# Kernel tuning notes

Measured on AMD Instinct MI355X. Metric: run time of the kernel, lower is better.

Reference implementation:

```python
import jax, jax.numpy as jnp
import numpy as np

# Winograd F(4x4, 3x3) transform matrices (wincnn convention, as in jiecaoyu/winograd)
BT = jnp.array([
    [4.,  0., -5.,  0., 1., 0.],
    [0., -4., -4.,  1., 1., 0.],
    [0.,  4., -4., -1., 1., 0.],
    [0., -2., -1.,  2., 1., 0.],
    [0.,  2., -1., -2., 1., 0.],
    [0.,  4.,  0., -5., 0., 1.]], dtype=jnp.float32)  # [6,6]
AT = jnp.array([
    [1., 1.,  1., 1.,  1., 0.],
    [0., 1., -1., 2., -2., 0.],
    [0., 1.,  1., 4.,  4., 0.],
    [0., 1., -1., 8., -8., 1.]], dtype=jnp.float32)  # [4,6]

KERNEL = 3
PAD = 1
GROUPS = 1
TILE_IN = 6   # input_tile_size
TILE_OUT = 4  # output_tile_size


def setup_inputs() -> dict:
    key = jax.random.key(0)
    k1, k2, k3 = jax.random.split(key, 3)
    N, Cin, H, W = 16, 64, 128, 128
    Cout = 64
    x = jax.random.normal(k1, (N, Cin, H, W), dtype=jnp.float32)
    # weight is stored in the Winograd (6x6 spectral) domain, as in the module
    weight = jax.random.normal(k2, (Cout, Cin // GROUPS, TILE_IN, TILE_IN), dtype=jnp.float32) * 0.01
    bias = jax.random.normal(k3, (Cout,), dtype=jnp.float32) * 0.01
    return {"x": x, "weight": weight, "bias": bias}


def reference(x, weight, bias):
    N, Cin, H0, W0 = x.shape
    Cout = weight.shape[0]
    g = GROUPS
    # conv padding
    x = jnp.pad(x, ((0, 0), (0, 0), (PAD, PAD), (PAD, PAD)))
    H = x.shape[2]
    out_w = H - KERNEL + 1
    # pad so output width is a multiple of the output tile size
    extra = (-out_w) % TILE_OUT
    if extra:
        x = jnp.pad(x, ((0, 0), (0, 0), (0, extra), (0, extra)))
    nt = (x.shape[2] - TILE_IN) // TILE_OUT + 1  # tiles per spatial dim
    # extract overlapping 6x6 tiles with stride 4 (the torch unfold)
    idx = jnp.arange(nt)[:, None] * TILE_OUT + jnp.arange(TILE_IN)[None, :]  # [nt,6]
    tiles = x[:, :, idx]                 # [N,C,nt,6,Wp]
    tiles = tiles[:, :, :, :, idx]       # [N,C,nt,6,nt,6]
    # input transform: V = BT @ d @ BT^T per tile -> [N,C,nt,nt,6,6]
    V = jnp.einsum('ai,ncpiqj,bj->ncpqab', BT, tiles, BT)
    # grouped spectral GEMM over input channels
    Vg = V.reshape(N, g, Cin // g, nt, nt, TILE_IN, TILE_IN)
    Wg = weight.reshape(g, Cout // g, Cin // g, TILE_IN, TILE_IN)
    M = jnp.einsum('goiab,ngipqab->ngopqab', Wg, Vg)
    M = M.reshape(N, Cout, nt, nt, TILE_IN, TILE_IN)
    # output transform: Y = AT @ M @ AT^T per tile -> [N,O,nt,nt,4,4]
    Y = jnp.einsum('xa,nopqab,yb->nopqxy', AT, M, AT)
    # stitch tiles back: [N,O,nt,4,nt,4] -> [N,O,nt*4,nt*4]
    y = Y.transpose(0, 1, 2, 4, 3, 5).reshape(N, Cout, nt * TILE_OUT, nt * TILE_OUT)
    y = y + bias[None, :, None, None]
    # crop the extra padding
    y = y[:, :, :out_w, :out_w]
    return y
```

## Files before the change

### kernel.cpp

```cpp
#include <hip/hip_runtime.h>
#include <stdint.h>

typedef __attribute__((ext_vector_type(4))) float f32x4;
typedef __attribute__((ext_vector_type(2))) float f32x2;
typedef __attribute__((ext_vector_type(8))) short s16x8;

#define WB_BYTES 294912

__device__ __forceinline__ short f2bf(float f) {
    uint32_t u = __builtin_bit_cast(uint32_t, f);
    u = u + 0x7FFFu + ((u >> 16) & 1u);
    return (short)(u >> 16);
}

__device__ __forceinline__ f32x4 load4u(const float* p) {
    f32x4 v;
    __builtin_memcpy(&v, p, 16);
    return v;
}

__global__ __launch_bounds__(256) void wtrans(const float* __restrict__ wf, short* __restrict__ wb) {
    int tid = blockIdx.x * 256 + threadIdx.x;
    const float* src = wf + tid * 36;
    float w[36];
#pragma unroll
    for (int i = 0; i < 9; i++) {
        f32x4 v = *(const f32x4*)(src + 4 * i);
        w[4*i+0] = v[0]; w[4*i+1] = v[1]; w[4*i+2] = v[2]; w[4*i+3] = v[3];
    }
#pragma unroll
    for (int ab = 0; ab < 36; ab++) wb[ab * 4096 + tid] = f2bf(w[ab]);
}

#define XCI 440
__global__ __launch_bounds__(1024) void wino_fused(const float* __restrict__ x,
                                                   const short* __restrict__ wb,
                                                   const float* __restrict__ bias,
                                                   float* __restrict__ out) {
    __shared__ __align__(16) float SM[39680];
    float* X0 = SM;
    float* X1 = SM + 14080;
    short* Vs = (short*)(SM + 28160);
    float* P0 = SM;
    float* P1 = SM + 16384;

    int t = threadIdx.x;
    int lane = t & 63;
    int w = t >> 6;
    int cog = w >> 2;
    int grp = w & 3;
    int sh = grp >> 1;
    int bh = grp & 1;
    int lo = lane & 15;
    int kq = lane >> 4;

    int ci_t = t & 31;
    int tl_t = (t >> 5) & 15;
    int s2_t = t >> 9;
    int tp = tl_t >> 2, tq = tl_t & 3;

    int tci[4], trow[4], tc4[4];
#pragma unroll
    for (int i = 0; i < 4; i++) {
        int s = i * 1024 + t;
        int ci = s / 108;
        int rem = s - ci * 108;
        int row = rem / 6;
        tci[i] = ci; trow[i] = row; tc4[i] = rem - row * 6;
    }
    bool v3 = t < 384;

    float bv = bias[cog * 16 + kq * 4 + grp];

    f32x4 acc[9];
#pragma unroll
    for (int i = 0; i < 9; i++) acc[i] = (f32x4){0.f, 0.f, 0.f, 0.f};

    f32x4 L[4];

    auto issueLoads = [&](int vb, int r) {
        int n = vb >> 6, sb = vb & 63;
        int row0 = (sb >> 3) * 16 - 1;
        int gc0 = (sb & 7) * 16 - 1;
        const float* xb = x + (size_t)n * 64 * 16384;
#pragma unroll
        for (int i = 0; i < 4; i++) {
            if (i < 3 || v3) {
                int gr = row0 + trow[i];
                int gc = gc0 + 4 * tc4[i];
                f32x4 v = (f32x4){0.f, 0.f, 0.f, 0.f};
                if ((unsigned)gr < 128u) {
                    const float* rowp = xb + (size_t)((r * 32 + tci[i]) * 128 + gr) * 128;
                    if (gc >= 0 && gc <= 124) {
                        v = load4u(rowp + gc);
                    } else {
                        if ((unsigned)(gc + 0) < 128u) v[0] = rowp[gc + 0];
                        if ((unsigned)(gc + 1) < 128u) v[1] = rowp[gc + 1];
                        if ((unsigned)(gc + 2) < 128u) v[2] = rowp[gc + 2];
                        if ((unsigned)(gc + 3) < 128u) v[3] = rowp[gc + 3];
                    }
                }
                L[i] = v;
            }
        }
    };

    auto writeX = [&](float* Xb) {
#pragma unroll
        for (int i = 0; i < 4; i++) {
            if (i < 3 || v3)
                *(f32x4*)&Xb[tci[i] * XCI + trow[i] * 24 + tc4[i] * 4] = L[i];
        }
    };

    auto transform = [&](const float* Xbuf) {
        const float* Xb = Xbuf + ci_t * XCI + tp * 96 + tq * 4;
        f32x4 ra[5]; f32x2 rb[5];
#pragma unroll
        for (int k = 0; k < 5; k++) {
            int off = (s2_t + k) * 24;
            ra[k] = *(const f32x4*)(Xb + off);
            rb[k] = *(const f32x2*)(Xb + off + 4);
        }
        float Ua[3][6];
#pragma unroll
        for (int c = 0; c < 6; c++) {
            float e0 = (c < 4) ? ra[0][c] : rb[0][c - 4];
            float e1 = (c < 4) ? ra[1][c] : rb[1][c - 4];
            float e2 = (c < 4) ? ra[2][c] : rb[2][c - 4];
            float e3 = (c < 4) ? ra[3][c] : rb[3][c - 4];
            float e4 = (c < 4) ? ra[4][c] : rb[4][c - 4];
            if (s2_t == 0) {
                float e = fmaf(-4.f, e2, e4);
                float f = fmaf(-4.f, e1, e3);
                Ua[0][c] = fmaf(4.f, e0 - e2, e4 - e2);
                Ua[1][c] = e + f;
                Ua[2][c] = e - f;
            } else {
                float g = e3 - e1;
                float h = e2 - e0;
                Ua[0][c] = fmaf(2.f, h, g);
                Ua[1][c] = fmaf(-2.f, h, g);
                Ua[2][c] = fmaf(4.f, e0 - e2, e4 - e2);
            }
        }
        short* vb = Vs + tl_t * 40 + ci_t;
#pragma unroll
        for (int ar = 0; ar < 3; ar++) {
            float m0 = Ua[ar][0], m1 = Ua[ar][1], m2 = Ua[ar][2];
            float m3 = Ua[ar][3], m4 = Ua[ar][4], m5 = Ua[ar][5];
            float e = fmaf(-4.f, m2, m4);
            float f = fmaf(-4.f, m1, m3);
            float g = m4 - m2;
            float h = m3 - m1;
            int base = (s2_t * 3 + ar) * 6;
            vb[(base + 0) * 640] = f2bf(fmaf(4.f, m0 - m2, g));
            vb[(base + 1) * 640] = f2bf(e + f);
            vb[(base + 2) * 640] = f2bf(e - f);
            vb[(base + 3) * 640] = f2bf(fmaf(2.f, h, g));
            vb[(base + 4) * 640] = f2bf(fmaf(-2.f, h, g));
            vb[(base + 5) * 640] = f2bf(fmaf(4.f, m1 - m3, m5 - m3));
        }
    };

    auto gemmStep = [&](int r) {
        const short* wb_base = wb + (cog * 16 + lo) * 64 + r * 32 + kq * 8;
        const short* v_base = Vs + lo * 40 + kq * 8;
#pragma unroll
        for (int ar = 0; ar < 3; ar++) {
#pragma unroll
            for (int br = 0; br < 3; br++) {
                int ab = (3 * sh + ar) * 6 + 3 * bh + br;
                s16x8 a0 = *(const s16x8*)(wb_base + ab * 4096);
                s16x8 b0 = *(const s16x8*)(v_base + ab * 640);
                acc[ar * 3 + br] = __builtin_amdgcn_mfma_f32_16x16x32_bf16(a0, b0, acc[ar * 3 + br], 0, 0, 0);
            }
        }
    };

    int vb0 = blockIdx.x * 4;
    issueLoads(vb0, 0);

    for (int it = 0; it < 4; ++it) {
        int vb = vb0 + it;
        int n = vb >> 6, sb = vb & 63;
        int p0_ = (sb >> 3) * 4;
        int q0_ = (sb & 7) * 4;

        writeX(X0);
        __syncthreads();
        issueLoads(vb, 1);
        transform(X0);
        writeX(X1);
        __syncthreads();
        gemmStep(0);
        __syncthreads();
        transform(X1);
        __syncthreads();
        gemmStep(1);
        __syncthreads();

        if (it < 3) issueLoads(vb + 1, 0);

        int p = p0_ + (lo >> 2);
        int q = q0_ + (lo & 3);
        float* Pown = (sh == 0) ? P0 : P1;

        if (bh == 0) {
#pragma unroll
            for (int rr = 0; rr < 4; rr++) {
                float z[4][3];
#pragma unroll
                for (int br = 0; br < 3; br++) {
                    float ma = acc[br][rr], mb = acc[3 + br][rr], mc = acc[6 + br][rr];
                    if (sh == 0) {
                        float s1 = mb + mc, d1 = mb - mc;
                        z[0][br] = ma + s1; z[1][br] = d1; z[2][br] = s1; z[3][br] = d1;
                    } else {
                        float sv = ma + mb, dv = ma - mb;
                        z[0][br] = sv; z[1][br] = 2.f * dv; z[2][br] = 4.f * sv;
                        z[3][br] = fmaf(8.f, dv, mc);
                    }
                }
#pragma unroll
                for (int xr = 0; xr < 4; xr++) {
                    float s1 = z[xr][1] + z[xr][2], d1 = z[xr][1] - z[xr][2];
                    f32x4 y;
                    y[0] = z[xr][0] + s1; y[1] = d1; y[2] = s1; y[3] = d1;
                    *(f32x4*)&Pown[cog * 4096 + (rr * 4 + xr) * 256 + lane * 4] = y;
                }
            }
        }
        __syncthreads();
        if (bh == 1) {
#pragma unroll
            for (int rr = 0; rr < 4; rr++) {
                float z[4][3];
#pragma unroll
                for (int br = 0; br < 3; br++) {
                    float ma = acc[br][rr], mb = acc[3 + br][rr], mc = acc[6 + br][rr];
                    if (sh == 0) {
                        float s1 = mb + mc, d1 = mb - mc;
                        z[0][br] = ma + s1; z[1][br] = d1; z[2][br] = s1; z[3][br] = d1;
                    } else {
                        float sv = ma + mb, dv = ma - mb;
                        z[0][br] = sv; z[1][br] = 2.f * dv; z[2][br] = 4.f * sv;
                        z[3][br] = fmaf(8.f, dv, mc);
                    }
                }
#pragma unroll
                for (int xr = 0; xr < 4; xr++) {
                    float s2 = z[xr][0] + z[xr][1], d2 = z[xr][0] - z[xr][1];
                    f32x4 y;
                    y[0] = s2; y[1] = 2.f * d2; y[2] = 4.f * s2;
                    y[3] = fmaf(8.f, d2, z[xr][2]);
                    float* pp = &Pown[cog * 4096 + (rr * 4 + xr) * 256 + lane * 4];
                    f32x4 old = *(const f32x4*)pp;
                    *(f32x4*)pp = old + y;
                }
            }
        }
        __syncthreads();
        {
            int rr = grp;
            int co = cog * 16 + kq * 4 + rr;
            float* ob = out + ((size_t)(n * 64 + co) * 128 + 4 * p) * 128 + 4 * q;
#pragma unroll
            for (int xr = 0; xr < 4; xr++) {
                int idx = cog * 4096 + (rr * 4 + xr) * 256 + lane * 4;
                f32x4 a0 = *(const f32x4*)&P0[idx];
                f32x4 a1 = *(const f32x4*)&P1[idx];
                f32x4 y;
                y[0] = a0[0] + a1[0] + bv;
                y[1] = a0[1] + a1[1] + bv;
                y[2] = a0[2] + a1[2] + bv;
                y[3] = a0[3] + a1[3] + bv;
                *(f32x4*)(ob + xr * 128) = y;
            }
        }
#pragma unroll
        for (int i = 0; i < 9; i++) acc[i] = (f32x4){0.f, 0.f, 0.f, 0.f};
        if (it < 3) __syncthreads();
    }
}

extern "C" void kernel_launch(void* const* d_in, const int* in_sizes, int n_in,
                              void* d_out, int out_size, void* d_ws, size_t ws_size,
                              hipStream_t stream) {
    const float* x    = (const float*)d_in[0];
    const float* wf   = (const float*)d_in[1];
    const float* bias = (const float*)d_in[2];
    float* out = (float*)d_out;

    if (ws_size < WB_BYTES) return;
    short* wb = (short*)d_ws;

    wtrans<<<16, 256, 0, stream>>>(wf, wb);
    wino_fused<<<256, 1024, 0, stream>>>(x, wb, bias, out);
}
```

Before: 224.1 us.

## One spatial block per workgroup, drop double-buffered prefetch, add interior fast path

New measurement: 187.1 us. -16.5%, faster.

```diff
diff --git a/kernel.cpp b/kernel.cpp
--- a/kernel.cpp
+++ b/kernel.cpp
@@ -32,15 +32,14 @@
     for (int ab = 0; ab < 36; ab++) wb[ab * 4096 + tid] = f2bf(w[ab]);
 }
 
-#define XCI 440
+#define XCI 436
 __global__ __launch_bounds__(1024) void wino_fused(const float* __restrict__ x,
                                                    const short* __restrict__ wb,
                                                    const float* __restrict__ bias,
                                                    float* __restrict__ out) {
-    __shared__ __align__(16) float SM[39680];
-    float* X0 = SM;
-    float* X1 = SM + 14080;
-    short* Vs = (short*)(SM + 28160);
+    __shared__ __align__(16) float SM[32768];
+    float* X = SM;
+    short* Vs = (short*)(SM + 13952);
     float* P0 = SM;
     float* P1 = SM + 16384;
 
@@ -59,16 +58,15 @@
     int s2_t = t >> 9;
     int tp = tl_t >> 2, tq = tl_t & 3;
 
-    int tci[4], trow[4], tc4[4];
-#pragma unroll
-    for (int i = 0; i < 4; i++) {
-        int s = i * 1024 + t;
-        int ci = s / 108;
-        int rem = s - ci * 108;
-        int row = rem / 6;
-        tci[i] = ci; trow[i] = row; tc4[i] = rem - row * 6;
-    }
-    bool v3 = t < 384;
+    int b = blockIdx.x;
+    int n = b >> 6, sb = b & 63;
+    int p0_ = (sb >> 3) * 4;
+    int q0_ = (sb & 7) * 4;
+    const float* xb = x + (size_t)n * 64 * 16384;
+    int row0 = 4 * p0_ - 1;
+    int gc0 = 4 * q0_ - 1;
+    int sr = sb >> 3, sc = sb & 7;
+    bool interior = (sr >= 1) & (sr <= 6) & (sc >= 1) & (sc <= 6);
 
     float bv = bias[cog * 16 + kq * 4 + grp];
 
@@ -76,211 +74,194 @@
 #pragma unroll
     for (int i = 0; i < 9; i++) acc[i] = (f32x4){0.f, 0.f, 0.f, 0.f};
 
-    f32x4 L[4];
-
-    auto issueLoads = [&](int vb, int r) {
-        int n = vb >> 6, sb = vb & 63;
-        int row0 = (sb >> 3) * 16 - 1;
-        int gc0 = (sb & 7) * 16 - 1;
-        const float* xb = x + (size_t)n * 64 * 16384;
-#pragma unroll
-        for (int i = 0; i < 4; i++) {
-            if (i < 3 || v3) {
-                int gr = row0 + trow[i];
-                int gc = gc0 + 4 * tc4[i];
-                f32x4 v = (f32x4){0.f, 0.f, 0.f, 0.f};
-                if ((unsigned)gr < 128u) {
-                    const float* rowp = xb + (size_t)((r * 32 + tci[i]) * 128 + gr) * 128;
-                    if (gc >= 0 && gc <= 124) {
-                        v = load4u(rowp + gc);
-                    } else {
-                        if ((unsigned)(gc + 0) < 128u) v[0] = rowp[gc + 0];
-                        if ((unsigned)(gc + 1) < 128u) v[1] = rowp[gc + 1];
-                        if ((unsigned)(gc + 2) < 128u) v[2] = rowp[gc + 2];
-                        if ((unsigned)(gc + 3) < 128u) v[3] = rowp[gc + 3];
+#pragma unroll
+    for (int r = 0; r < 2; r++) {
+        const float* xrb = xb + (size_t)r * 32 * 16384;
+        if (interior) {
+#pragma unroll
+            for (int i = 0; i < 4; i++) {
+                if (i < 3 || t < 384) {
+                    int s = i * 1024 + t;
+                    int ci = s / 108;
+                    int rem = s - ci * 108;
+                    int row = rem / 6;
+                    int c4 = rem - row * 6;
+                    f32x4 v = load4u(xrb + (size_t)(ci * 128 + row0 + row) * 128 + (gc0 + 4 * c4));
+                    *(f32x4*)&X[ci * XCI + row * 24 + c4 * 4] = v;
+                }
+            }
+        } else {
+#pragma unroll
+            for (int i = 0; i < 4; i++) {
+                if (i < 3 || t < 384) {
+                    int s = i * 1024 + t;
+                    int ci = s / 108;
+                    int rem = s - ci * 108;
+                    int row = rem / 6;
+                    int c4 = rem - row * 6;
+                    int gr = row0 + row;
+                    int gc = gc0 + 4 * c4;
+                    f32x4 v = (f32x4){0.f, 0.f, 0.f, 0.f};
+                    if ((unsigned)gr < 128u) {
+                        const float* rowp = xrb + (size_t)(ci * 128 + gr) * 128;
+                        if (gc >= 0 && gc <= 124) {
+                            v = load4u(rowp + gc);
+                        } else {
+                            if ((unsigned)(gc + 0) < 128u) v[0] = rowp[gc + 0];
+                            if ((unsigned)(gc + 1) < 128u) v[1] = rowp[gc + 1];
+                            if ((unsigned)(gc + 2) < 128u) v[2] = rowp[gc + 2];
+                            if ((unsigned)(gc + 3) < 128u) v[3] = rowp[gc + 3];
+                        }
                     }
-                }
-                L[i] = v;
-            }
-        }
-    };
-
-    auto writeX = [&](float* Xb) {
-#pragma unroll
-        for (int i = 0; i < 4; i++) {
-            if (i < 3 || v3)
-                *(f32x4*)&Xb[tci[i] * XCI + trow[i] * 24 + tc4[i] * 4] = L[i];
-        }
-    };
-
-    auto transform = [&](const float* Xbuf) {
-        const float* Xb = Xbuf + ci_t * XCI + tp * 96 + tq * 4;
-        f32x4 ra[5]; f32x2 rb[5];
-#pragma unroll
-        for (int k = 0; k < 5; k++) {
-            int off = (s2_t + k) * 24;
-            ra[k] = *(const f32x4*)(Xb + off);
-            rb[k] = *(const f32x2*)(Xb + off + 4);
-        }
-        float Ua[3][6];
-#pragma unroll
-        for (int c = 0; c < 6; c++) {
-            float e0 = (c < 4) ? ra[0][c] : rb[0][c - 4];
-            float e1 = (c < 4) ? ra[1][c] : rb[1][c - 4];
-            float e2 = (c < 4) ? ra[2][c] : rb[2][c - 4];
-            float e3 = (c < 4) ? ra[3][c] : rb[3][c - 4];
-            float e4 = (c < 4) ? ra[4][c] : rb[4][c - 4];
-            if (s2_t == 0) {
-                float e = fmaf(-4.f, e2, e4);
-                float f = fmaf(-4.f, e1, e3);
-                Ua[0][c] = fmaf(4.f, e0 - e2, e4 - e2);
-                Ua[1][c] = e + f;
-                Ua[2][c] = e - f;
-            } else {
-                float g = e3 - e1;
-                float h = e2 - e0;
-                Ua[0][c] = fmaf(2.f, h, g);
-                Ua[1][c] = fmaf(-2.f, h, g);
-                Ua[2][c] = fmaf(4.f, e0 - e2, e4 - e2);
-            }
-        }
-        short* vb = Vs + tl_t * 40 + ci_t;
-#pragma unroll
-        for (int ar = 0; ar < 3; ar++) {
-            float m0 = Ua[ar][0], m1 = Ua[ar][1], m2 = Ua[ar][2];
-            float m3 = Ua[ar][3], m4 = Ua[ar][4], m5 = Ua[ar][5];
-            float e = fmaf(-4.f, m2, m4);
-            float f = fmaf(-4.f, m1, m3);
-            float g = m4 - m2;
-            float h = m3 - m1;
-            int base = (s2_t * 3 + ar) * 6;
-            vb[(base + 0) * 640] = f2bf(fmaf(4.f, m0 - m2, g));
-            vb[(base + 1) * 640] = f2bf(e + f);
-            vb[(base + 2) * 640] = f2bf(e - f);
-            vb[(base + 3) * 640] = f2bf(fmaf(2.f, h, g));
-            vb[(base + 4) * 640] = f2bf(fmaf(-2.f, h, g));
-            vb[(base + 5) * 640] = f2bf(fmaf(4.f, m1 - m3, m5 - m3));
-        }
-    };
-
-    auto gemmStep = [&](int r) {
-        const short* wb_base = wb + (cog * 16 + lo) * 64 + r * 32 + kq * 8;
-        const short* v_base = Vs + lo * 40 + kq * 8;
-#pragma unroll
-        for (int ar = 0; ar < 3; ar++) {
+                    *(f32x4*)&X[ci * XCI + row * 24 + c4 * 4] = v;
+                }
+            }
+        }
+        __syncthreads();
+
+        {
+            const float* Xb = X + ci_t * XCI + tp * 96 + tq * 4;
+            f32x4 ra[5]; f32x2 rb[5];
+#pragma unroll
+            for (int k = 0; k < 5; k++) {
+                int off = (s2_t + k) * 24;
+                ra[k] = *(const f32x4*)(Xb + off);
+                rb[k] = *(const f32x2*)(Xb + off + 4);
+            }
+            float Ua[3][6];
+#pragma unroll
+            for (int c = 0; c < 6; c++) {
+                float e0 = (c < 4) ? ra[0][c] : rb[0][c - 4];
+                float e1 = (c < 4) ? ra[1][c] : rb[1][c - 4];
+                float e2 = (c < 4) ? ra[2][c] : rb[2][c - 4];
+                float e3 = (c < 4) ? ra[3][c] : rb[3][c - 4];
+                float e4 = (c < 4) ? ra[4][c] : rb[4][c - 4];
+                if (s2_t == 0) {
+                    float e = fmaf(-4.f, e2, e4);
+                    float f = fmaf(-4.f, e1, e3);
+                    Ua[0][c] = fmaf(4.f, e0 - e2, e4 - e2);
+                    Ua[1][c] = e + f;
+                    Ua[2][c] = e - f;
+                } else {
+                    float g = e3 - e1;
+                    float h = e2 - e0;
+                    Ua[0][c] = fmaf(2.f, h, g);
+                    Ua[1][c] = fmaf(-2.f, h, g);
+                    Ua[2][c] = fmaf(4.f, e0 - e2, e4 - e2);
+                }
+            }
+            short* vb = Vs + tl_t * 40 + ci_t;
+#pragma unroll
+            for (int ar = 0; ar < 3; ar++) {
+                float m0 = Ua[ar][0], m1 = Ua[ar][1], m2 = Ua[ar][2];
+                float m3 = Ua[ar][3], m4 = Ua[ar][4], m5 = Ua[ar][5];
+                float e = fmaf(-4.f, m2, m4);
+                float f = fmaf(-4.f, m1, m3);
+                float g = m4 - m2;
+                float h = m3 - m1;
+                int base = (s2_t * 3 + ar) * 6;
+                vb[(base + 0) * 640] = f2bf(fmaf(4.f, m0 - m2, g));
+                vb[(base + 1) * 640] = f2bf(e + f);
+                vb[(base + 2) * 640] = f2bf(e - f);
+                vb[(base + 3) * 640] = f2bf(fmaf(2.f, h, g));
+                vb[(base + 4) * 640] = f2bf(fmaf(-2.f, h, g));
+                vb[(base + 5) * 640] = f2bf(fmaf(4.f, m1 - m3, m5 - m3));
+            }
+        }
+        __syncthreads();
+
+        {
+            const short* wb_base = wb + (cog * 16 + lo) * 64 + r * 32 + kq * 8;
+            const short* v_base = Vs + lo * 40 + kq * 8;
+#pragma unroll
+            for (int ar = 0; ar < 3; ar++) {
+#pragma unroll
+                for (int br = 0; br < 3; br++) {
+                    int ab = (3 * sh + ar) * 6 + 3 * bh + br;
+                    s16x8 a0 = *(const s16x8*)(wb_base + ab * 4096);
+                    s16x8 b0 = *(const s16x8*)(v_base + ab * 640);
+                    acc[ar * 3 + br] = __builtin_amdgcn_mfma_f32_16x16x32_bf16(a0, b0, acc[ar * 3 + br], 0, 0, 0);
+                }
+            }
+        }
+    }
+
+    __syncthreads();
+    int p = p0_ + (lo >> 2);
+    int q = q0_ + (lo & 3);
+    float* Pown = (sh == 0) ? P0 : P1;
+
+    if (bh == 0) {
+#pragma unroll
+        for (int rr = 0; rr < 4; rr++) {
+            float z[4][3];
 #pragma unroll
             for (int br = 0; br < 3; br++) {
-                int ab = (3 * sh + ar) * 6 + 3 * bh + br;
-                s16x8 a0 = *(const s16x8*)(wb_base + ab * 4096);
-                s16x8 b0 = *(const s16x8*)(v_base + ab * 640);
-                acc[ar * 3 + br] = __builtin_amdgcn_mfma_f32_16x16x32_bf16(a0, b0, acc[ar * 3 + br], 0, 0, 0);
-            }
-        }
-    };
-
-    int vb0 = blockIdx.x * 4;
-    issueLoads(vb0, 0);
-
-    for (int it = 0; it < 4; ++it) {
-        int vb = vb0 + it;
-        int n = vb >> 6, sb = vb & 63;
-        int p0_ = (sb >> 3) * 4;
-        int q0_ = (sb & 7) * 4;
-
-        writeX(X0);
-        __syncthreads();
-        issueLoads(vb, 1);
-        transform(X0);
-        writeX(X1);
-        __syncthreads();
-        gemmStep(0);
-        __syncthreads();
-        transform(X1);
-        __syncthreads();
-        gemmStep(1);
-        __syncthreads();
-
-        if (it < 3) issueLoads(vb + 1, 0);
-
-        int p = p0_ + (lo >> 2);
-        int q = q0_ + (lo & 3);
-        float* Pown = (sh == 0) ? P0 : P1;
-
-        if (bh == 0) {
-#pragma unroll
-            for (int rr = 0; rr < 4; rr++) {
-                float z[4][3];
-#pragma unroll
-                for (int br = 0; br < 3; br++) {
-                    float ma = acc[br][rr], mb = acc[3 + br][rr], mc = acc[6 + br][rr];
-                    if (sh == 0) {
-                        float s1 = mb + mc, d1 = mb - mc;
-                        z[0][br] = ma + s1; z[1][br] = d1; z[2][br] = s1; z[3][br] = d1;
-                    } else {
-                        float sv = ma + mb, dv = ma - mb;
-                        z[0][br] = sv; z[1][br] = 2.f * dv; z[2][br] = 4.f * sv;
-                        z[3][br] = fmaf(8.f, dv, mc);
-                    }
-                }
-#pragma unroll
-                for (int xr = 0; xr < 4; xr++) {
-                    float s1 = z[xr][1] + z[xr][2], d1 = z[xr][1] - z[xr][2];
-                    f32x4 y;
-                    y[0] = z[xr][0] + s1; y[1] = d1; y[2] = s1; y[3] = d1;
-                    *(f32x4*)&Pown[cog * 4096 + (rr * 4 + xr) * 256 + lane * 4] = y;
-                }
-            }
-        }
-        __syncthreads();
-        if (bh == 1) {
-#pragma unroll
-            for (int rr = 0; rr < 4; rr++) {
-                float z[4][3];
-#pragma unroll
-                for (int br = 0; br < 3; br++) {
-                    float ma = acc[br][rr], mb = acc[3 + br][rr], mc = acc[6 + br][rr];
-                    if (sh == 0) {
-                        float s1 = mb + mc, d1 = mb - mc;
-                        z[0][br] = ma + s1; z[1][br] = d1; z[2][br] = s1; z[3][br] = d1;
-                    } else {
-                        float sv = ma + mb, dv = ma - mb;
-                        z[0][br] = sv; z[1][br] = 2.f * dv; z[2][br] = 4.f * sv;
-                        z[3][br] = fmaf(8.f, dv, mc);
-                    }
-                }
-#pragma unroll
-                for (int xr = 0; xr < 4; xr++) {
-                    float s2 = z[xr][0] + z[xr][1], d2 = z[xr][0] - z[xr][1];
-                    f32x4 y;
-                    y[0] = s2; y[1] = 2.f * d2; y[2] = 4.f * s2;
-                    y[3] = fmaf(8.f, d2, z[xr][2]);
-                    float* pp = &Pown[cog * 4096 + (rr * 4 + xr) * 256 + lane * 4];
-                    f32x4 old = *(const f32x4*)pp;
-                    *(f32x4*)pp = old + y;
-                }
-            }
-        }
-        __syncthreads();
-        {
-            int rr = grp;
-            int co = cog * 16 + kq * 4 + rr;
-            float* ob = out + ((size_t)(n * 64 + co) * 128 + 4 * p) * 128 + 4 * q;
+                float ma = acc[br][rr], mb = acc[3 + br][rr], mc = acc[6 + br][rr];
+                if (sh == 0) {
+                    float s1 = mb + mc, d1 = mb - mc;
+                    z[0][br] = ma + s1; z[1][br] = d1; z[2][br] = s1; z[3][br] = d1;
+                } else {
+                    float sv = ma + mb, dv = ma - mb;
+                    z[0][br] = sv; z[1][br] = 2.f * dv; z[2][br] = 4.f * sv;
+                    z[3][br] = fmaf(8.f, dv, mc);
+                }
+            }
 #pragma unroll
             for (int xr = 0; xr < 4; xr++) {
-                int idx = cog * 4096 + (rr * 4 + xr) * 256 + lane * 4;
-                f32x4 a0 = *(const f32x4*)&P0[idx];
-                f32x4 a1 = *(const f32x4*)&P1[idx];
+                float s1 = z[xr][1] + z[xr][2], d1 = z[xr][1] - z[xr][2];
                 f32x4 y;
-                y[0] = a0[0] + a1[0] + bv;
-                y[1] = a0[1] + a1[1] + bv;
-                y[2] = a0[2] + a1[2] + bv;
-                y[3] = a0[3] + a1[3] + bv;
-                *(f32x4*)(ob + xr * 128) = y;
-            }
-        }
-#pragma unroll
-        for (int i = 0; i < 9; i++) acc[i] = (f32x4){0.f, 0.f, 0.f, 0.f};
-        if (it < 3) __syncthreads();
+                y[0] = z[xr][0] + s1; y[1] = d1; y[2] = s1; y[3] = d1;
+                *(f32x4*)&Pown[cog * 4096 + (rr * 4 + xr) * 256 + lane * 4] = y;
+            }
+        }
+    }
+    __syncthreads();
+    if (bh == 1) {
+#pragma unroll
+        for (int rr = 0; rr < 4; rr++) {
+            float z[4][3];
+#pragma unroll
+            for (int br = 0; br < 3; br++) {
+                float ma = acc[br][rr], mb = acc[3 + br][rr], mc = acc[6 + br][rr];
+                if (sh == 0) {
+                    float s1 = mb + mc, d1 = mb - mc;
+                    z[0][br] = ma + s1; z[1][br] = d1; z[2][br] = s1; z[3][br] = d1;
+                } else {
+                    float sv = ma + mb, dv = ma - mb;
+                    z[0][br] = sv; z[1][br] = 2.f * dv; z[2][br] = 4.f * sv;
+                    z[3][br] = fmaf(8.f, dv, mc);
+                }
+            }
+#pragma unroll
+            for (int xr = 0; xr < 4; xr++) {
+                float s2 = z[xr][0] + z[xr][1], d2 = z[xr][0] - z[xr][1];
+                f32x4 y;
+                y[0] = s2; y[1] = 2.f * d2; y[2] = 4.f * s2;
+                y[3] = fmaf(8.f, d2, z[xr][2]);
+                float* pp = &Pown[cog * 4096 + (rr * 4 + xr) * 256 + lane * 4];
+                f32x4 old = *(const f32x4*)pp;
+                *(f32x4*)pp = old + y;
+            }
+        }
+    }
+    __syncthreads();
+    {
+        int rr = grp;
+        int co = cog * 16 + kq * 4 + rr;
+        float* ob = out + ((size_t)(n * 64 + co) * 128 + 4 * p) * 128 + 4 * q;
+#pragma unroll
+        for (int xr = 0; xr < 4; xr++) {
+            int idx = cog * 4096 + (rr * 4 + xr) * 256 + lane * 4;
+            f32x4 a0 = *(const f32x4*)&P0[idx];
+            f32x4 a1 = *(const f32x4*)&P1[idx];
+            f32x4 y;
+            y[0] = a0[0] + a1[0] + bv;
+            y[1] = a0[1] + a1[1] + bv;
+            y[2] = a0[2] + a1[2] + bv;
+            y[3] = a0[3] + a1[3] + bv;
+            *(f32x4*)(ob + xr * 128) = y;
+        }
     }
 }
 
@@ -296,5 +277,5 @@
     short* wb = (short*)d_ws;
 
     wtrans<<<16, 256, 0, stream>>>(wf, wb);
-    wino_fused<<<256, 1024, 0, stream>>>(x, wb, bias, out);
-}
+    wino_fused<<<1024, 1024, 0, stream>>>(x, wb, bias, out);
+}
```
